# Kernel optimization log

Hardware: AMD Instinct MI355X
Metric: run time of the kernel (lower is better)

The kernel has to match this reference:

```python
import jax, jax.numpy as jnp
import numpy as np
import math

B, D, K = 256, 128, 4096
OUTPUT_SIZE = 1281167
T = 0.07


def setup_inputs() -> dict:
    key = jax.random.key(0)
    k1, k2, k3, k4 = jax.random.split(key, 4)
    x = jax.random.normal(k1, (B, D), dtype=jnp.float32)
    y = jax.random.randint(k2, (B,), 0, OUTPUT_SIZE, dtype=jnp.int64)
    idx = jax.random.randint(k3, (B, K + 1), 0, OUTPUT_SIZE, dtype=jnp.int64)
    stdv = 1.0 / math.sqrt(D / 3.0)
    memory = jax.random.uniform(k4, (OUTPUT_SIZE, D), dtype=jnp.float32,
                                minval=-stdv, maxval=stdv)
    return {"x": x, "y": y, "idx": idx, "memory": memory}


def reference(x, y, idx, memory):
    outputSize = memory.shape[0]
    # first column of idx is overwritten with the positive index y
    idx = idx.at[:, 0].set(y)
    # gather K+1 rows per sample from the memory bank: (B, K+1, D)
    weight = memory[idx]
    # batched dot product: (B, K+1)
    logits = jnp.einsum('bkd,bd->bk', weight, x) / T
    e = jnp.exp(logits)
    # Z is set on first call from the batch statistics (params[2] == -1 path)
    Z = e.mean() * outputSize
    out = e / Z
    return out
```

## Files before the change

### kernel.cpp

```cpp
#include <hip/hip_runtime.h>


constexpr int   kB          = 256;
constexpr int   kKp1        = 4097;
constexpr long long kOutRows = 1281167LL;
constexpr int   kSplits     = 8;
constexpr int   kMainBlocks = kB * kSplits;
constexpr int   kThreads    = 256;
constexpr float kInvT       = 1.0f / 0.07f;

__device__ __forceinline__ float dot4(float4 a, float4 b) {
    return a.x * b.x + a.y * b.y + a.z * b.z + a.w * b.w;
}

__global__ __launch_bounds__(kThreads) void nce_main(
    const float* __restrict__ x, const int* __restrict__ y,
    const int* __restrict__ idx, const float* __restrict__ memory,
    float* __restrict__ out, float* __restrict__ blksum)
{
    const int b     = blockIdx.x >> 3;
    const int chunk = blockIdx.x & 7;
    const int tid   = threadIdx.x;
    const int wave  = tid >> 6;
    const int lane  = tid & 63;
    const int half  = lane >> 5;
    const int dlane = lane & 31;
    const int g     = wave * 2 + half;

    const float4 xv = reinterpret_cast<const float4*>(x)[b * 32 + dlane];
    const float4* m4   = reinterpret_cast<const float4*>(memory);
    const int*    idxb = idx + (size_t)b * kKp1;
    float*        outb = out + (size_t)b * kKp1;
    const int     ypos = y[b];

    const int per = (kKp1 + kSplits - 1) / kSplits;
    const int k0  = chunk * per;
    const int k1  = (k0 + per < kKp1) ? (k0 + per) : kKp1;

    float acc = 0.0f;
    for (int kb = k0 + g * 4; kb < k1; kb += 32) {
        const int krem = k1 - kb;
        const int r0 = (kb == 0) ? ypos : idxb[kb];
        const int r1 = (krem > 1) ? idxb[kb + 1] : 0;
        const int r2 = (krem > 2) ? idxb[kb + 2] : 0;
        const int r3 = (krem > 3) ? idxb[kb + 3] : 0;
        const float4 a0 = m4[(size_t)r0 * 32 + dlane];
        const float4 a1 = m4[(size_t)r1 * 32 + dlane];
        const float4 a2 = m4[(size_t)r2 * 32 + dlane];
        const float4 a3 = m4[(size_t)r3 * 32 + dlane];
        float d0 = dot4(a0, xv), d1 = dot4(a1, xv);
        float d2 = dot4(a2, xv), d3 = dot4(a3, xv);
        #pragma unroll
        for (int m = 16; m >= 1; m >>= 1) {
            d0 += __shfl_xor(d0, m, 64);
            d1 += __shfl_xor(d1, m, 64);
            d2 += __shfl_xor(d2, m, 64);
            d3 += __shfl_xor(d3, m, 64);
        }
        if (dlane == 0) {
            const float e0 = __expf(d0 * kInvT);
            const float e1 = __expf(d1 * kInvT);
            const float e2 = __expf(d2 * kInvT);
            const float e3 = __expf(d3 * kInvT);
            outb[kb] = e0;  acc += e0;
            if (krem > 1) { outb[kb + 1] = e1; acc += e1; }
            if (krem > 2) { outb[kb + 2] = e2; acc += e2; }
            if (krem > 3) { outb[kb + 3] = e3; acc += e3; }
        }
    }

    #pragma unroll
    for (int m = 32; m >= 1; m >>= 1)
        acc += __shfl_xor(acc, m, 64);
    __shared__ float red[kThreads / 64];
    if (lane == 0) red[wave] = acc;
    __syncthreads();
    if (tid == 0)
        blksum[blockIdx.x] = red[0] + red[1] + red[2] + red[3];
}

__global__ __launch_bounds__(256) void nce_norm(
    float4* __restrict__ out4, const float* __restrict__ blksum, int n4)
{
    float s = 0.0f;
    for (int i = threadIdx.x; i < kMainBlocks; i += 256) s += blksum[i];
    #pragma unroll
    for (int m = 32; m >= 1; m >>= 1)
        s += __shfl_xor(s, m, 64);
    __shared__ float red[4];
    if ((threadIdx.x & 63) == 0) red[threadIdx.x >> 6] = s;
    __syncthreads();
    const float tot = red[0] + red[1] + red[2] + red[3];
    const float sc = ((float)(kB * kKp1) / (float)kOutRows) / tot;

    int i = blockIdx.x * blockDim.x + threadIdx.x;
    const int stride = gridDim.x * blockDim.x;
    for (; i < n4; i += stride) {
        float4 v = out4[i];
        v.x *= sc; v.y *= sc; v.z *= sc; v.w *= sc;
        out4[i] = v;
    }
}

extern "C" void kernel_launch(void* const* d_in, const int* in_sizes, int n_in,
                              void* d_out, int out_size, void* d_ws, size_t ws_size,
                              hipStream_t stream) {
    const float* x      = (const float*)d_in[0];
    const int*   y      = (const int*)d_in[1];
    const int*   idx    = (const int*)d_in[2];
    const float* memory = (const float*)d_in[3];
    float*       out    = (float*)d_out;
    float*       blksum = (float*)d_ws;

    hipLaunchKernelGGL(nce_main, dim3(kMainBlocks), dim3(kThreads), 0, stream,
                       x, y, idx, memory, out, blksum);
    hipLaunchKernelGGL(nce_norm, dim3(1024), dim3(256), 0, stream,
                       (float4*)d_out, blksum, out_size / 4);
}
```

Before: 91.21 us.

## Fuse normalization into main kernel using cooperative grid sync

Merges the gather/dot/exp kernel and the normalization kernel into one cooperative kernel. After each block writes its partial sum it does a grid-wide sync, sums all partials, and rescales only its own chunk of outputs. This removes the second launch and the full re-read of the output from a separate pass. In exchange it adds grid-sync overhead, a per-call occupancy query on the host, and a grid sized to fit co-resident blocks, which may reduce parallelism.

```diff
diff --git a/kernel.cpp b/kernel.cpp
--- a/kernel.cpp
+++ b/kernel.cpp
@@ -1,39 +1,40 @@
 #include <hip/hip_runtime.h>
+#include <hip/hip_cooperative_groups.h>
+
+namespace cg = cooperative_groups;
 
 
-constexpr int   kB          = 256;
-constexpr int   kKp1        = 4097;
+constexpr int       kB       = 256;
+constexpr int       kKp1     = 4097;
 constexpr long long kOutRows = 1281167LL;
-constexpr int   kSplits     = 8;
-constexpr int   kMainBlocks = kB * kSplits;
-constexpr int   kThreads    = 256;
-constexpr float kInvT       = 1.0f / 0.07f;
+constexpr int       kThreads = 256;
+constexpr float     kInvT    = 1.0f / 0.07f;
 
 __device__ __forceinline__ float dot4(float4 a, float4 b) {
     return a.x * b.x + a.y * b.y + a.z * b.z + a.w * b.w;
 }
 
-__global__ __launch_bounds__(kThreads) void nce_main(
+__global__ __launch_bounds__(kThreads) void nce_fused(
     const float* __restrict__ x, const int* __restrict__ y,
     const int* __restrict__ idx, const float* __restrict__ memory,
-    float* __restrict__ out, float* __restrict__ blksum)
+    float* __restrict__ out, float* __restrict__ blksum, int chunksPerB)
 {
-    const int b     = blockIdx.x >> 3;
-    const int chunk = blockIdx.x & 7;
+    const int nBlocks = gridDim.x;
+    const int b     = blockIdx.x / chunksPerB;
+    const int chunk = blockIdx.x % chunksPerB;
     const int tid   = threadIdx.x;
     const int wave  = tid >> 6;
     const int lane  = tid & 63;
-    const int half  = lane >> 5;
     const int dlane = lane & 31;
-    const int g     = wave * 2 + half;
+    const int g     = wave * 2 + (lane >> 5);
 
-    const float4 xv = reinterpret_cast<const float4*>(x)[b * 32 + dlane];
+    const float4  xv   = reinterpret_cast<const float4*>(x)[b * 32 + dlane];
     const float4* m4   = reinterpret_cast<const float4*>(memory);
     const int*    idxb = idx + (size_t)b * kKp1;
     float*        outb = out + (size_t)b * kKp1;
     const int     ypos = y[b];
 
-    const int per = (kKp1 + kSplits - 1) / kSplits;
+    const int per = (kKp1 + chunksPerB - 1) / chunksPerB;
     const int k0  = chunk * per;
     const int k1  = (k0 + per < kKp1) ? (k0 + per) : kKp1;
 
@@ -75,31 +76,26 @@
     __shared__ float red[kThreads / 64];
     if (lane == 0) red[wave] = acc;
     __syncthreads();
-    if (tid == 0)
+    if (tid == 0) {
         blksum[blockIdx.x] = red[0] + red[1] + red[2] + red[3];
-}
+        __threadfence();
+    }
 
-__global__ __launch_bounds__(256) void nce_norm(
-    float4* __restrict__ out4, const float* __restrict__ blksum, int n4)
-{
+    cg::this_grid().sync();
+
     float s = 0.0f;
-    for (int i = threadIdx.x; i < kMainBlocks; i += 256) s += blksum[i];
+    for (int i = tid; i < nBlocks; i += kThreads) s += blksum[i];
     #pragma unroll
     for (int m = 32; m >= 1; m >>= 1)
         s += __shfl_xor(s, m, 64);
-    __shared__ float red[4];
-    if ((threadIdx.x & 63) == 0) red[threadIdx.x >> 6] = s;
+    __shared__ float red2[kThreads / 64];
+    if (lane == 0) red2[wave] = s;
     __syncthreads();
-    const float tot = red[0] + red[1] + red[2] + red[3];
+    const float tot = red2[0] + red2[1] + red2[2] + red2[3];
     const float sc = ((float)(kB * kKp1) / (float)kOutRows) / tot;
 
-    int i = blockIdx.x * blockDim.x + threadIdx.x;
-    const int stride = gridDim.x * blockDim.x;
-    for (; i < n4; i += stride) {
-        float4 v = out4[i];
-        v.x *= sc; v.y *= sc; v.z *= sc; v.w *= sc;
-        out4[i] = v;
-    }
+    for (int k = k0 + tid; k < k1; k += kThreads)
+        outb[k] *= sc;
 }
 
 extern "C" void kernel_launch(void* const* d_in, const int* in_sizes, int n_in,
@@ -112,8 +108,17 @@
     float*       out    = (float*)d_out;
     float*       blksum = (float*)d_ws;
 
-    hipLaunchKernelGGL(nce_main, dim3(kMainBlocks), dim3(kThreads), 0, stream,
-                       x, y, idx, memory, out, blksum);
-    hipLaunchKernelGGL(nce_norm, dim3(1024), dim3(256), 0, stream,
-                       (float4*)d_out, blksum, out_size / 4);
+    int maxPerCU = 0;
+    (void)hipOccupancyMaxActiveBlocksPerMultiprocessor(
+        &maxPerCU, (const void*)nce_fused, kThreads, 0);
+    if (maxPerCU < 1) maxPerCU = 1;
+    int chunksPerB = (maxPerCU * 256) / kB;
+    if (chunksPerB > 8) chunksPerB = 8;
+    if (chunksPerB < 1) chunksPerB = 1;
+    const int nBlocks = kB * chunksPerB;
+
+    void* args[] = { (void*)&x, (void*)&y, (void*)&idx, (void*)&memory,
+                     (void*)&out, (void*)&blksum, (void*)&chunksPerB };
+    (void)hipLaunchCooperativeKernel((const void*)nce_fused, dim3(nBlocks),
+                                     dim3(kThreads), args, 0, stream);
 }
```

New measurement: 295.5 us. 224% more time.
